# Performance work log

Measured on AMD Instinct MI355X. Metric: run time of the kernel, lower is better.

The kernel has to match this reference:

```python
import jax, jax.numpy as jnp
import numpy as np

N_HEADS = 8
WINDOW = 64
NEG = -1e9


def _layer_norm(x, g, b, eps=1e-5):
    mu = jnp.mean(x, axis=-1, keepdims=True)
    var = jnp.mean((x - mu) ** 2, axis=-1, keepdims=True)
    return g * (x - mu) / jnp.sqrt(var + eps) + b


def _sinusoidal_pe(S, D):
    pos = jnp.arange(S, dtype=jnp.float32)[:, None]
    div = jnp.exp(jnp.arange(0, D, 2, dtype=jnp.float32) * (-jnp.log(jnp.float32(10000.0)) / D))
    pe = jnp.zeros((S, D), jnp.float32)
    pe = pe.at[:, 0::2].set(jnp.sin(pos * div))
    pe = pe.at[:, 1::2].set(jnp.cos(pos * div))
    return pe


def setup_inputs():
    key = jax.random.key(0)
    ks = jax.random.split(key, 8)
    L, S, D, DFF = 4, 2048, 1024, 2048
    p = lambda k, shape: jax.random.normal(k, shape, jnp.float32) * 0.02
    return {
        "T": 1800,
        "enc_inputs": jax.random.normal(ks[0], (1, S, D), jnp.float32),
        "global_idx": jax.random.randint(ks[1], (32,), 0, 27000),
        "Wq": p(ks[2], (L, D, D)),
        "Wk": p(ks[3], (L, D, D)),
        "Wv": p(ks[4], (L, D, D)),
        "Wo": p(ks[5], (L, D, D)),
        "ln1_g": jnp.ones((L, D), jnp.float32),
        "ln1_b": jnp.zeros((L, D), jnp.float32),
        "W1": p(ks[6], (L, D, DFF)),
        "W2": p(ks[7], (L, DFF, D)),
        "ln2_g": jnp.ones((L, D), jnp.float32),
        "ln2_b": jnp.zeros((L, D), jnp.float32),
    }


def reference(T, enc_inputs, global_idx, Wq, Wk, Wv, Wo, ln1_g, ln1_b, W1, W2, ln2_g, ln2_b):
    B, S, D = enc_inputs.shape
    L = Wq.shape[0]
    H, DK = N_HEADS, D // N_HEADS

    # enc_outputs = enc_inputs + PE(enc_inputs) = 2*enc_inputs + pe (faithful to source)
    pe = _sinusoidal_pe(S, D)
    x = enc_inputs + (enc_inputs + pe[None])

    # mask vector: 1 = local token, -1 = global token, 0 = pad
    idx = jnp.arange(S)
    mvec = jnp.where(idx < T, 1.0, 0.0)
    g = global_idx // 15
    valid = (g >= 0) & (g < S)
    is_global = jnp.any((idx[None, :] == g[:, None]) & valid[:, None], axis=0)
    mvec = jnp.where(is_global, jnp.float32(-1.0), mvec)

    half = WINDOW // 2
    local = jnp.abs(idx[:, None] - idx[None, :]) <= half
    nonpad = mvec != 0.0
    glob = mvec == -1.0
    allowed = nonpad[:, None] & nonpad[None, :] & (local | glob[:, None] | glob[None, :])
    scale = 1.0 / jnp.sqrt(jnp.float32(DK))

    for l in range(L):
        # local-global multi-head self-attention
        q = (x @ Wq[l]).reshape(B, S, H, DK).transpose(0, 2, 1, 3)
        k = (x @ Wk[l]).reshape(B, S, H, DK).transpose(0, 2, 1, 3)
        v = (x @ Wv[l]).reshape(B, S, H, DK).transpose(0, 2, 1, 3)
        scores = jnp.einsum("bhqd,bhkd->bhqk", q, k) * scale
        scores = jnp.where(allowed[None, None], scores, jnp.float32(NEG))
        attn = jax.nn.softmax(scores, axis=-1)
        ctx = jnp.einsum("bhqk,bhkd->bhqd", attn, v).transpose(0, 2, 1, 3).reshape(B, S, D)
        x = _layer_norm(ctx @ Wo[l] + x, ln1_g[l], ln1_b[l])
        # position-wise FFN with residual + LayerNorm
        h = jax.nn.relu(x @ W1[l]) @ W2[l]
        x = _layer_norm(h + x, ln2_g[l], ln2_b[l])

    return x[0]  # squeeze(0): (S, D)
```

## Files before the change

### kernel.cpp

```cpp
#include <hip/hip_runtime.h>
#include <cstdint>
#include <cstddef>

#define S_LEN  2048
#define D_MODEL 1024
#define D_FF   2048
#define NLAYER 4

typedef float  f32x4  __attribute__((ext_vector_type(4)));
typedef __bf16 bf16x8 __attribute__((ext_vector_type(8)));
typedef __bf16 bf16x4 __attribute__((ext_vector_type(4)));

#define ATT_SCALE 0.08838834764831845f

__device__ __forceinline__ void async_copy16(const void* g, void* s) {
    __builtin_amdgcn_global_load_lds((const __attribute__((address_space(1))) void*)g,
                                     (__attribute__((address_space(3))) void*)s, 16, 0, 0);
}

template<int NW>
__device__ __forceinline__ float blockRedSum(float v, float* red) {
    #pragma unroll
    for (int off = 32; off > 0; off >>= 1) v += __shfl_down(v, off);
    const int t = threadIdx.x;
    if ((t & 63) == 0) red[t >> 6] = v;
    __syncthreads();
    float r = red[0];
    #pragma unroll
    for (int i = 1; i < NW; i++) r += red[i];
    __syncthreads();
    return r;
}

__global__ __launch_bounds__(256)
void init_mask_kernel(const float* __restrict__ enc, float* __restrict__ x,
                      __bf16* __restrict__ xb, const int* __restrict__ gidx,
                      int* __restrict__ isg, int* __restrict__ gcols, int* __restrict__ ngc,
                      float* __restrict__ vmean) {
    const int t = threadIdx.x;
    if (blockIdx.x < S_LEN) {
        const int s = blockIdx.x;
        #pragma unroll
        for (int i = 0; i < 4; i++) {
            const int d = t + i * 256;
            const float freq = expf(-(float)(d & ~1) * (9.210340371976184f / 1024.0f));
            const float ang = (float)s * freq;
            const float pe = (d & 1) ? cosf(ang) : sinf(ang);
            const float v = 2.0f * enc[(size_t)s * D_MODEL + d] + pe;
            x[(size_t)s * D_MODEL + d] = v;
            xb[(size_t)s * D_MODEL + d] = (__bf16)v;
        }
    } else {
        #pragma unroll
        for (int i = 0; i < 4; i++) vmean[t + i * 256] = 0.0f;
        __shared__ int gsh[32];
        __shared__ int cnt;
        if (t < 32) {
            const int g = gidx[t] / 15;
            gsh[t] = (g >= 0 && g < S_LEN) ? g : -1;
        }
        if (t == 0) cnt = 0;
        __syncthreads();
        #pragma unroll
        for (int i = 0; i < 8; i++) {
            const int s = t + i * 256;
            int f = 0;
            #pragma unroll
            for (int j = 0; j < 32; j++) f |= (gsh[j] == s) ? 1 : 0;
            isg[s] = f;
            if (f) { const int p = atomicAdd(&cnt, 1); gcols[p] = s; }
        }
        __syncthreads();
        if (t == 0) *ngc = cnt;
    }
}

__global__ __launch_bounds__(256)
void transpose_all_kernel(const float* __restrict__ Wq, const float* __restrict__ Wk,
                          const float* __restrict__ Wv, const float* __restrict__ Wo,
                          const float* __restrict__ W1, const float* __restrict__ W2,
                          __bf16* __restrict__ out) {
    const int layer = blockIdx.x >> 10;
    const int r = blockIdx.x & 1023;
    const size_t lw = (size_t)layer * 1024 * 1024;
    const size_t lf = (size_t)layer * 1024 * 2048;
    __bf16* arena = out + (size_t)layer * 8 * 1024 * 1024;
    const float* in; __bf16* o; int K, N, n0, k0;
    if (r < 512) {
        const int m = r >> 7, rr = r & 127;
        in = ((m == 0) ? Wq : (m == 1) ? Wk : (m == 2) ? Wv : Wo) + lw;
        o  = arena + (size_t)m * 1024 * 1024;
        K = 1024; N = 1024; n0 = (rr & 7) * 128; k0 = (rr >> 3) * 64;
    } else if (r < 768) {
        const int rr = r - 512;
        in = W1 + lf; o = arena + (size_t)4 * 1024 * 1024;
        K = 1024; N = 2048; n0 = (rr & 15) * 128; k0 = (rr >> 4) * 64;
    } else {
        const int rr = r - 768;
        in = W2 + lf; o = arena + (size_t)6 * 1024 * 1024;
        K = 2048; N = 1024; n0 = (rr & 7) * 128; k0 = (rr >> 3) * 64;
    }
    __shared__ __bf16 tile[128][80];
    const int t = threadIdx.x;
    {
        const int n4 = t & 31;
        const int kg = t >> 5;
        #pragma unroll
        for (int u = 0; u < 2; u++) {
            const int k4 = kg + 8 * u;
            f32x4 v[4];
            #pragma unroll
            for (int kk = 0; kk < 4; kk++)
                v[kk] = *(const f32x4*)&in[(size_t)(k0 + 4 * k4 + kk) * N + n0 + 4 * n4];
            const int cpr = ((k4 >> 1) ^ (n4 & 7)) * 2 + (k4 & 1);
            #pragma unroll
            for (int j = 0; j < 4; j++) {
                bf16x4 w;
                w[0] = (__bf16)v[0][j];
                w[1] = (__bf16)v[1][j];
                w[2] = (__bf16)v[2][j];
                w[3] = (__bf16)v[3][j];
                *(bf16x4*)&tile[4 * n4 + j][4 * cpr] = w;
            }
        }
    }
    __syncthreads();
    {
        const int p = t & 7, nb = t >> 3;
        #pragma unroll
        for (int i = 0; i < 4; i++) {
            const int n = nb + 32 * i;
            const bf16x8 vv = *(const bf16x8*)&tile[n][8 * (p ^ ((n >> 2) & 7))];
            *(bf16x8*)&o[(size_t)(n0 + n) * K + k0 + 8 * p] = vv;
        }
    }
}

template<int BM, int BN, int WSM, int WSN, int EPI, bool VACC>
__global__ __launch_bounds__(WSM * WSN * 64)
void gemm_bt(const __bf16* __restrict__ A, const __bf16* __restrict__ Bt,
             void* __restrict__ Cv, float* __restrict__ vmean, int M, int N, int K) {
    constexpr int NW = WSM * WSN, NT = NW * 64;
    constexpr int WM = BM / WSM, WN = BN / WSN;
    constexpr int MI = WM / 16, NI = WN / 16;
    constexpr int RPR = NT / 8;
    constexpr int RA = BM / RPR, RB = BN / RPR;
    __shared__ __bf16 As[2 * BM * 64];
    __shared__ __bf16 Bs[2 * BN * 64];
    const int t = threadIdx.x;
    const int w = t >> 6, l = t & 63;
    const int l15 = l & 15, q4 = l >> 4;
    const int wr = w / WSN, wc = w % WSN;
    const int m0 = blockIdx.y * BM, n0 = blockIdx.x * BN;

    const int srow = t >> 3;
    const int kc8  = (((t & 7) ^ (srow & 7)) * 8);
    const __bf16* ag = A  + (size_t)(m0 + srow) * K + kc8;
    const __bf16* bg = Bt + (size_t)(n0 + srow) * K + kc8;

    const int r7 = l15 & 7;
    int arow[MI], brow[NI];
    #pragma unroll
    for (int i = 0; i < MI; i++) arow[i] = (wr * WM + i * 16 + l15) * 64;
    #pragma unroll
    for (int j = 0; j < NI; j++) brow[j] = (wc * WN + j * 16 + l15) * 64;

    f32x4 acc[MI][NI];
    #pragma unroll
    for (int i = 0; i < MI; i++)
        #pragma unroll
        for (int j = 0; j < NI; j++) acc[i][j] = (f32x4){0.f, 0.f, 0.f, 0.f};

    auto stage = [&](int buf, int k0) {
        __bf16* ab = As + buf * (BM * 64) + w * 512;
        __bf16* bb = Bs + buf * (BN * 64) + w * 512;
        #pragma unroll
        for (int rr = 0; rr < RA; rr++)
            async_copy16(ag + (size_t)rr * RPR * K + k0, ab + rr * RPR * 64);
        #pragma unroll
        for (int rr = 0; rr < RB; rr++)
            async_copy16(bg + (size_t)rr * RPR * K + k0, bb + rr * RPR * 64);
    };
    auto compute = [&](int buf) {
        const __bf16* ab = As + buf * (BM * 64);
        const __bf16* bb = Bs + buf * (BN * 64);
        #pragma unroll
        for (int s = 0; s < 64; s += 32) {
            const int slot = ((q4 + (s >> 3)) ^ r7) * 8;
            bf16x8 af[MI], bfr[NI];
            #pragma unroll
            for (int i = 0; i < MI; i++) af[i]  = *(const bf16x8*)(ab + arow[i] + slot);
            #pragma unroll
            for (int j = 0; j < NI; j++) bfr[j] = *(const bf16x8*)(bb + brow[j] + slot);
            #pragma unroll
            for (int i = 0; i < MI; i++)
                #pragma unroll
                for (int j = 0; j < NI; j++)
                    acc[i][j] = __builtin_amdgcn_mfma_f32_16x16x32_bf16(af[i], bfr[j], acc[i][j], 0, 0, 0);
        }
    };

    stage(0, 0);
    __syncthreads();
    int cur = 0;
    int k0 = 0;
    for (; k0 + 64 < K; k0 += 64) {
        stage(cur ^ 1, k0 + 64);
        compute(cur);
        __syncthreads();
        cur ^= 1;
    }
    compute(cur);

    const int r0 = m0 + wr * WM + q4 * 4;
    const int c0 = n0 + wc * WN + l15;
    if constexpr (EPI == 0) {
        float* C = (float*)Cv;
        #pragma unroll
        for (int i = 0; i < MI; i++)
            #pragma unroll
            for (int j = 0; j < NI; j++)
                #pragma unroll
                for (int r = 0; r < 4; r++)
                    C[(size_t)(r0 + i * 16 + r) * N + c0 + j * 16] = acc[i][j][r];
    } else if constexpr (EPI == 1) {
        __bf16* C = (__bf16*)Cv;
        #pragma unroll
        for (int i = 0; i < MI; i++)
            #pragma unroll
            for (int j = 0; j < NI; j++)
                #pragma unroll
                for (int r = 0; r < 4; r++)
                    C[(size_t)(r0 + i * 16 + r) * N + c0 + j * 16] = (__bf16)fmaxf(acc[i][j][r], 0.0f);
    } else {
        __bf16* C = (__bf16*)Cv;
        #pragma unroll
        for (int i = 0; i < MI; i++)
            #pragma unroll
            for (int j = 0; j < NI; j++)
                #pragma unroll
                for (int r = 0; r < 4; r++)
                    C[(size_t)(r0 + i * 16 + r) * N + c0 + j * 16] = (__bf16)acc[i][j][r];
    }
    if constexpr (VACC) {
        #pragma unroll
        for (int j = 0; j < NI; j++) {
            const int col = c0 + j * 16;
            if (col >= 2048) {
                float s = 0.f;
                #pragma unroll
                for (int i = 0; i < MI; i++)
                    #pragma unroll
                    for (int r = 0; r < 4; r++) s += acc[i][j][r];
                s += __shfl_xor(s, 16);
                s += __shfl_xor(s, 32);
                if (q4 == 0) atomicAdd(&vmean[col - 2048], s);
            }
        }
    }
}

__global__ __launch_bounds__(256)
void attn_kernel(const __bf16* __restrict__ qkvb, const int* __restrict__ Tp,
                 const int* __restrict__ isg, const int* __restrict__ gcols,
                 const int* __restrict__ ngcp, const float* __restrict__ vmean,
                 __bf16* __restrict__ ctx, float* __restrict__ Og,
                 float* __restrict__ mg, float* __restrict__ lg) {
    const int h = blockIdx.y, hd = h * 128;
    const int t = threadIdx.x;
    const int T = *Tp, ng = *ngcp;
    __shared__ __bf16 Qs[32 * 136];
    __shared__ __bf16 Ks[128 * 136];
    __shared__ __bf16 Vs[128 * 136];
    __shared__ __bf16 Ps[32 * 136];
    __shared__ float  Ss[32 * 129];
    __shared__ int cix[128], cgf[128], rtype[32];
    __shared__ int ncs;
    const int l = t & 63, w = t >> 6;
    const int l15 = l & 15, q4 = l >> 4;
    const int nb = w * 32;

    if (blockIdx.x < 64) {
        const int qt0 = blockIdx.x * 32;
        const int wl = max(qt0 - 32, 0), wh = min(qt0 + 63, S_LEN - 1);
        if (t == 0) ncs = 0;
        if (t < 32) { const int qr = qt0 + t; rtype[t] = isg[qr] ? 1 : (qr < T ? 0 : 2); }
        __syncthreads();
        if (t <= wh - wl) {
            const int c = wl + t, gf = isg[c];
            if (c < T || gf) { const int p = atomicAdd(&ncs, 1); cix[p] = c; cgf[p] = gf; }
        }
        if (t < ng) {
            const int c = gcols[t];
            if (c < wl || c > wh) { const int p = atomicAdd(&ncs, 1); cix[p] = c; cgf[p] = 1; }
        }
        {
            const int r = t >> 3, d0 = (t & 7) * 16;
            const bf16x8* src = (const bf16x8*)(qkvb + (size_t)(qt0 + r) * 3072 + hd + d0);
            *(bf16x8*)&Qs[r * 136 + d0]     = src[0];
            *(bf16x8*)&Qs[r * 136 + d0 + 8] = src[1];
        }
        __syncthreads();
        const int nc = ncs;
        if (nc + t < 128) { cix[nc + t] = -1; cgf[nc + t] = 0; }
        {
            const int j = t >> 1, d0 = (t & 1) * 64;
            const int ci = (j < nc) ? cix[j] : -1;
            if (ci >= 0) {
                const bf16x8* kp = (const bf16x8*)(qkvb + (size_t)ci * 3072 + 1024 + hd + d0);
                const bf16x8* vp = (const bf16x8*)(qkvb + (size_t)ci * 3072 + 2048 + hd + d0);
                #pragma unroll
                for (int i = 0; i < 8; i++) {
                    *(bf16x8*)&Ks[j * 136 + d0 + i * 8] = kp[i];
                    *(bf16x8*)&Vs[j * 136 + d0 + i * 8] = vp[i];
                }
            } else {
                #pragma unroll
                for (int i = 0; i < 8; i++) {
                    *(bf16x8*)&Ks[j * 136 + d0 + i * 8] = (bf16x8)(__bf16)0.f;
                    *(bf16x8*)&Vs[j * 136 + d0 + i * 8] = (bf16x8)(__bf16)0.f;
                }
            }
        }
        __syncthreads();
        {
            f32x4 sacc[2][2];
            #pragma unroll
            for (int i = 0; i < 2; i++)
                #pragma unroll
                for (int j = 0; j < 2; j++) sacc[i][j] = (f32x4){0.f, 0.f, 0.f, 0.f};
            #pragma unroll
            for (int kk = 0; kk < 4; kk++) {
                const int k0 = kk * 32;
                bf16x8 af[2], bk[2];
                af[0] = *(const bf16x8*)&Qs[l15 * 136 + k0 + q4 * 8];
                af[1] = *(const bf16x8*)&Qs[(16 + l15) * 136 + k0 + q4 * 8];
                bk[0] = *(const bf16x8*)&Ks[(nb + l15) * 136 + k0 + q4 * 8];
                bk[1] = *(const bf16x8*)&Ks[(nb + 16 + l15) * 136 + k0 + q4 * 8];
                #pragma unroll
                for (int m2 = 0; m2 < 2; m2++)
                    #pragma unroll
                    for (int n2 = 0; n2 < 2; n2++)
                        sacc[m2][n2] = __builtin_amdgcn_mfma_f32_16x16x32_bf16(af[m2], bk[n2], sacc[m2][n2], 0, 0, 0);
            }
            #pragma unroll
            for (int m2 = 0; m2 < 2; m2++)
                #pragma unroll
                for (int n2 = 0; n2 < 2; n2++)
                    #pragma unroll
                    for (int r = 0; r < 4; r++) {
                        const int row = m2 * 16 + q4 * 4 + r;
                        const int col = nb + n2 * 16 + l15;
                        const int c = cix[col];
                        const int dd = qt0 + row - c;
                        const bool ok = (c >= 0) && (((unsigned)(dd + 32) <= 64u) || cgf[col]);
                        Ss[row * 129 + col] = ok ? sacc[m2][n2][r] * ATT_SCALE : -1e30f;
                    }
        }
        __syncthreads();
        {
            const int r = t >> 3, i = t & 7;
            float mx = -1e30f;
            for (int c = i; c < 128; c += 8) mx = fmaxf(mx, Ss[r * 129 + c]);
            #pragma unroll
            for (int off = 4; off > 0; off >>= 1) mx = fmaxf(mx, __shfl_down(mx, off, 8));
            mx = __shfl(mx, 0, 8);
            float sm = 0.f;
            for (int c = i; c < 128; c += 8) {
                const float s = Ss[r * 129 + c];
                const float p = (s > -1e29f) ? __expf(s - mx) : 0.f;
                Ss[r * 129 + c] = p;
                sm += p;
            }
            #pragma unroll
            for (int off = 4; off > 0; off >>= 1) sm += __shfl_down(sm, off, 8);
            sm = __shfl(sm, 0, 8);
            const float rl = 1.0f / fmaxf(sm, 1e-30f);
            for (int c = i; c < 128; c += 8) Ps[r * 136 + c] = (__bf16)(Ss[r * 129 + c] * rl);
        }
        __syncthreads();
        {
            f32x4 oacc[2][2];
            #pragma unroll
            for (int i = 0; i < 2; i++)
                #pragma unroll
                for (int j = 0; j < 2; j++) oacc[i][j] = (f32x4){0.f, 0.f, 0.f, 0.f};
            #pragma unroll
            for (int kk = 0; kk < 4; kk++) {
                const int k0 = kk * 32;
                bf16x8 ap[2], bv[2];
                ap[0] = *(const bf16x8*)&Ps[l15 * 136 + k0 + q4 * 8];
                ap[1] = *(const bf16x8*)&Ps[(16 + l15) * 136 + k0 + q4 * 8];
                #pragma unroll
                for (int n2 = 0; n2 < 2; n2++) {
                    const int dimn = nb + n2 * 16 + l15;
                    #pragma unroll
                    for (int jj = 0; jj < 8; jj++)
                        bv[n2][jj] = Vs[(k0 + q4 * 8 + jj) * 136 + dimn];
                }
                #pragma unroll
                for (int m2 = 0; m2 < 2; m2++)
                    #pragma unroll
                    for (int n2 = 0; n2 < 2; n2++)
                        oacc[m2][n2] = __builtin_amdgcn_mfma_f32_16x16x32_bf16(ap[m2], bv[n2], oacc[m2][n2], 0, 0, 0);
            }
            #pragma unroll
            for (int m2 = 0; m2 < 2; m2++)
                #pragma unroll
                for (int n2 = 0; n2 < 2; n2++)
                    #pragma unroll
                    for (int r = 0; r < 4; r++) {
                        const int row = m2 * 16 + q4 * 4 + r;
                        const int dim = nb + n2 * 16 + l15;
                        const int rt = rtype[row];
                        const size_t o = (size_t)(qt0 + row) * D_MODEL + hd + dim;
                        if (rt == 0)      ctx[o] = (__bf16)oacc[m2][n2][r];
                        else if (rt == 2) ctx[o] = (__bf16)(vmean[hd + dim] * (1.0f / 2048.0f));
                    }
        }
    } else {
        if (ng == 0) return;
        const int cb = blockIdx.x - 64, c0 = cb * 128;
        {
            const int r = t >> 3, d0 = (t & 7) * 16;
            if (r < ng) {
                const bf16x8* src = (const bf16x8*)(qkvb + (size_t)gcols[r] * 3072 + hd + d0);
                *(bf16x8*)&Qs[r * 136 + d0]     = src[0];
                *(bf16x8*)&Qs[r * 136 + d0 + 8] = src[1];
            } else {
                *(bf16x8*)&Qs[r * 136 + d0]     = (bf16x8)(__bf16)0.f;
                *(bf16x8*)&Qs[r * 136 + d0 + 8] = (bf16x8)(__bf16)0.f;
            }
        }
        if (t < 128) { const int c = c0 + t; cix[t] = (c < T || isg[c]) ? 1 : 0; }
        {
            const int j = t >> 1, d0 = (t & 1) * 64;
            const int ci = c0 + j;
            const bf16x8* kp = (const bf16x8*)(qkvb + (size_t)ci * 3072 + 1024 + hd + d0);
            const bf16x8* vp = (const bf16x8*)(qkvb + (size_t)ci * 3072 + 2048 + hd + d0);
            #pragma unroll
            for (int i = 0; i < 8; i++) {
                *(bf16x8*)&Ks[j * 136 + d0 + i * 8] = kp[i];
                *(bf16x8*)&Vs[j * 136 + d0 + i * 8] = vp[i];
            }
        }
        __syncthreads();
        {
            f32x4 sacc[2][2];
            #pragma unroll
            for (int i = 0; i < 2; i++)
                #pragma unroll
                for (int j = 0; j < 2; j++) sacc[i][j] = (f32x4){0.f, 0.f, 0.f, 0.f};
            #pragma unroll
            for (int kk = 0; kk < 4; kk++) {
                const int k0 = kk * 32;
                bf16x8 af[2], bk[2];
                af[0] = *(const bf16x8*)&Qs[l15 * 136 + k0 + q4 * 8];
                af[1] = *(const bf16x8*)&Qs[(16 + l15) * 136 + k0 + q4 * 8];
                bk[0] = *(const bf16x8*)&Ks[(nb + l15) * 136 + k0 + q4 * 8];
                bk[1] = *(const bf16x8*)&Ks[(nb + 16 + l15) * 136 + k0 + q4 * 8];
                #pragma unroll
                for (int m2 = 0; m2 < 2; m2++)
                    #pragma unroll
                    for (int n2 = 0; n2 < 2; n2++)
                        sacc[m2][n2] = __builtin_amdgcn_mfma_f32_16x16x32_bf16(af[m2], bk[n2], sacc[m2][n2], 0, 0, 0);
            }
            #pragma unroll
            for (int m2 = 0; m2 < 2; m2++)
                #pragma unroll
                for (int n2 = 0; n2 < 2; n2++)
                    #pragma unroll
                    for (int r = 0; r < 4; r++) {
                        const int row = m2 * 16 + q4 * 4 + r;
                        const int col = nb + n2 * 16 + l15;
                        Ss[row * 129 + col] = cix[col] ? sacc[m2][n2][r] * ATT_SCALE : -1e30f;
                    }
        }
        __syncthreads();
        {
            const int r = t >> 3, i = t & 7;
            float mx = -1e30f;
            for (int c = i; c < 128; c += 8) mx = fmaxf(mx, Ss[r * 129 + c]);
            #pragma unroll
            for (int off = 4; off > 0; off >>= 1) mx = fmaxf(mx, __shfl_down(mx, off, 8));
            mx = __shfl(mx, 0, 8);
            float sm = 0.f;
            for (int c = i; c < 128; c += 8) {
                const float s = Ss[r * 129 + c];
                const float p = (s > -1e29f) ? __expf(s - mx) : 0.f;
                Ps[r * 136 + c] = (__bf16)p;
                sm += p;
            }
            #pragma unroll
            for (int off = 4; off > 0; off >>= 1) sm += __shfl_down(sm, off, 8);
            if (i == 0) { mg[(h * 16 + cb) * 32 + r] = mx; lg[(h * 16 + cb) * 32 + r] = sm; }
        }
        __syncthreads();
        {
            f32x4 oacc[2][2];
            #pragma unroll
            for (int i = 0; i < 2; i++)
                #pragma unroll
                for (int j = 0; j < 2; j++) oacc[i][j] = (f32x4){0.f, 0.f, 0.f, 0.f};
            #pragma unroll
            for (int kk = 0; kk < 4; kk++) {
                const int k0 = kk * 32;
                bf16x8 ap[2], bv[2];
                ap[0] = *(const bf16x8*)&Ps[l15 * 136 + k0 + q4 * 8];
                ap[1] = *(const bf16x8*)&Ps[(16 + l15) * 136 + k0 + q4 * 8];
                #pragma unroll
                for (int n2 = 0; n2 < 2; n2++) {
                    const int dimn = nb + n2 * 16 + l15;
                    #pragma unroll
                    for (int jj = 0; jj < 8; jj++)
                        bv[n2][jj] = Vs[(k0 + q4 * 8 + jj) * 136 + dimn];
                }
                #pragma unroll
                for (int m2 = 0; m2 < 2; m2++)
                    #pragma unroll
                    for (int n2 = 0; n2 < 2; n2++)
                        oacc[m2][n2] = __builtin_amdgcn_mfma_f32_16x16x32_bf16(ap[m2], bv[n2], oacc[m2][n2], 0, 0, 0);
            }
            #pragma unroll
            for (int m2 = 0; m2 < 2; m2++)
                #pragma unroll
                for (int n2 = 0; n2 < 2; n2++)
                    #pragma unroll
                    for (int r = 0; r < 4; r++) {
                        const int row = m2 * 16 + q4 * 4 + r;
                        const int dim = nb + n2 * 16 + l15;
                        Og[((size_t)(h * 16 + cb) * 32 + row) * 128 + dim] = oacc[m2][n2][r];
                    }
        }
    }
}

__global__ __launch_bounds__(256)
void attn_gcomb(const int* __restrict__ gcols, const int* __restrict__ ngcp,
                const float* __restrict__ Og, const float* __restrict__ mg,
                const float* __restrict__ lg, __bf16* __restrict__ ctx) {
    const int h = blockIdx.x, hd = h * 128, t = threadIdx.x;
    const int ng = *ngcp;
    const int r = t >> 3, i = t & 7;
    if (r >= ng) return;
    float M = -1e30f;
    #pragma unroll
    for (int cb = 0; cb < 16; cb++) M = fmaxf(M, mg[(h * 16 + cb) * 32 + r]);
    float e[16], L = 0.f;
    #pragma unroll
    for (int cb = 0; cb < 16; cb++) {
        e[cb] = __expf(mg[(h * 16 + cb) * 32 + r] - M);
        L += e[cb] * lg[(h * 16 + cb) * 32 + r];
    }
    const float rL = 1.0f / fmaxf(L, 1e-30f);
    const int grow = gcols[r];
    for (int d = i; d < 128; d += 8) {
        float o = 0.f;
        #pragma unroll
        for (int cb = 0; cb < 16; cb++)
            o += e[cb] * Og[((size_t)(h * 16 + cb) * 32 + r) * 128 + d];
        ctx[(size_t)grow * D_MODEL + hd + d] = (__bf16)(o * rL);
    }
}

__global__ __launch_bounds__(256)
void ln_kernel(const float* __restrict__ y, const float* __restrict__ r,
               const float* __restrict__ g, const float* __restrict__ b,
               float* __restrict__ xo, __bf16* __restrict__ xb, float* __restrict__ vz) {
    const int row = blockIdx.x, t = threadIdx.x;
    if (vz != nullptr && row == 0) {
        #pragma unroll
        for (int i = 0; i < 4; i++) vz[t + i * 256] = 0.0f;
    }
    const float* yr = y + (size_t)row * D_MODEL;
    const float* rr = r + (size_t)row * D_MODEL;
    __shared__ float red[4];
    float v[4]; float s = 0.f;
    #pragma unroll
    for (int i = 0; i < 4; i++) { const int d = t + i * 256; v[i] = yr[d] + rr[d]; s += v[i]; }
    s = blockRedSum<4>(s, red);
    const float mu = s * (1.0f / 1024.0f);
    float vs = 0.f;
    #pragma unroll
    for (int i = 0; i < 4; i++) { const float dd = v[i] - mu; vs += dd * dd; }
    vs = blockRedSum<4>(vs, red);
    const float rstd = rsqrtf(vs * (1.0f / 1024.0f) + 1e-5f);
    #pragma unroll
    for (int i = 0; i < 4; i++) {
        const int d = t + i * 256;
        const float o = g[d] * (v[i] - mu) * rstd + b[d];
        xo[(size_t)row * D_MODEL + d] = o;
        xb[(size_t)row * D_MODEL + d] = (__bf16)o;
    }
}

extern "C" void kernel_launch(void* const* d_in, const int* in_sizes, int n_in,
                              void* d_out, int out_size, void* d_ws, size_t ws_size,
                              hipStream_t stream) {
    const int*   Tp   = (const int*)  d_in[0];
    const float* enc  = (const float*)d_in[1];
    const int*   gidx = (const int*)  d_in[2];
    const float* Wq   = (const float*)d_in[3];
    const float* Wk   = (const float*)d_in[4];
    const float* Wv   = (const float*)d_in[5];
    const float* Wo   = (const float*)d_in[6];
    const float* ln1g = (const float*)d_in[7];
    const float* ln1b = (const float*)d_in[8];
    const float* W1   = (const float*)d_in[9];
    const float* W2   = (const float*)d_in[10];
    const float* ln2g = (const float*)d_in[11];
    const float* ln2b = (const float*)d_in[12];

    char* p = (char*)d_ws;
    size_t off = 0;
    auto alloc = [&](size_t bytes) -> void* {
        void* q = p + off;
        off += (bytes + 255) & ~(size_t)255;
        return q;
    };
    float*  x     = (float*) alloc((size_t)S_LEN * D_MODEL * 4);
    __bf16* xb    = (__bf16*)alloc((size_t)S_LEN * D_MODEL * 2);
    __bf16* qkvb  = (__bf16*)alloc((size_t)S_LEN * 3072 * 2);
    __bf16* ctx   = (__bf16*)alloc((size_t)S_LEN * D_MODEL * 2);
    float*  g1    = (float*) alloc((size_t)S_LEN * D_MODEL * 4);
    __bf16* h1    = (__bf16*)alloc((size_t)S_LEN * D_FF * 2);
    __bf16* wT    = (__bf16*)alloc((size_t)4 * 8 * 1024 * 1024 * 2);
    float*  vmean = (float*) alloc(1024 * 4);
    int*    isg   = (int*)   alloc(S_LEN * 4);
    int*    gcols = (int*)   alloc(S_LEN * 4);
    int*    ngc   = (int*)   alloc(256);
    float*  Og    = (float*) alloc((size_t)8 * 16 * 32 * 128 * 4);
    float*  mgb   = (float*) alloc(8 * 16 * 32 * 4);
    float*  lgb   = (float*) alloc(8 * 16 * 32 * 4);

    init_mask_kernel<<<S_LEN + 1, 256, 0, stream>>>(enc, x, xb, gidx, isg, gcols, ngc, vmean);
    transpose_all_kernel<<<4096, 256, 0, stream>>>(Wq, Wk, Wv, Wo, W1, W2, wT);

    for (int l = 0; l < NLAYER; l++) {
        __bf16* wL = wT + (size_t)l * 8 * 1024 * 1024;
        gemm_bt<64, 128, 1, 2, 2, true><<<dim3(24, 32), 128, 0, stream>>>(xb, wL, (void*)qkvb, vmean, S_LEN, 3072, 1024);

        attn_kernel<<<dim3(80, 8), 256, 0, stream>>>(qkvb, Tp, isg, gcols, ngc, vmean, ctx, Og, mgb, lgb);
        attn_gcomb<<<8, 256, 0, stream>>>(gcols, ngc, Og, mgb, lgb, ctx);

        gemm_bt<64, 64, 2, 2, 0, false><<<dim3(16, 32), 256, 0, stream>>>(ctx, wL + (size_t)3 * 1024 * 1024, (void*)g1, nullptr, S_LEN, 1024, 1024);
        ln_kernel<<<S_LEN, 256, 0, stream>>>(g1, x, ln1g + l * 1024, ln1b + l * 1024, x, xb, nullptr);

        gemm_bt<64, 128, 2, 2, 1, false><<<dim3(16, 32), 256, 0, stream>>>(xb, wL + (size_t)4 * 1024 * 1024, (void*)h1, nullptr, S_LEN, 2048, 1024);
        gemm_bt<64, 64, 2, 2, 0, false><<<dim3(16, 32), 256, 0, stream>>>(h1, wL + (size_t)6 * 1024 * 1024, (void*)g1, nullptr, S_LEN, 1024, 2048);
        float* xout = (l == NLAYER - 1) ? (float*)d_out : x;
        ln_kernel<<<S_LEN, 256, 0, stream>>>(g1, x, ln2g + l * 1024, ln2b + l * 1024, xout, xb, vmean);
    }
}
```

Baseline: 702.8 us.

## Keep Q and softmax scores in registers in attention; widen QKV GEMM block

```diff
diff --git a/kernel.cpp b/kernel.cpp
--- a/kernel.cpp
+++ b/kernel.cpp
@@ -269,19 +269,24 @@
     const int h = blockIdx.y, hd = h * 128;
     const int t = threadIdx.x;
     const int T = *Tp, ng = *ngcp;
-    __shared__ __bf16 Qs[32 * 136];
     __shared__ __bf16 Ks[128 * 136];
     __shared__ __bf16 Vs[128 * 136];
     __shared__ __bf16 Ps[32 * 136];
-    __shared__ float  Ss[32 * 129];
+    __shared__ float  wmax[4 * 32];
+    __shared__ float  wsum[4 * 32];
     __shared__ int cix[128], cgf[128], rtype[32];
     __shared__ int ncs;
     const int l = t & 63, w = t >> 6;
     const int l15 = l & 15, q4 = l >> 4;
     const int nb = w * 32;
 
-    if (blockIdx.x < 64) {
-        const int qt0 = blockIdx.x * 32;
+    const bool isLocal = (blockIdx.x < 64);
+    if (!isLocal && ng == 0) return;
+
+    bf16x8 qreg[2][4];
+    int qt0 = 0, cb = 0;
+    if (isLocal) {
+        qt0 = blockIdx.x * 32;
         const int wl = max(qt0 - 32, 0), wh = min(qt0 + 63, S_LEN - 1);
         if (t == 0) ncs = 0;
         if (t < 32) { const int qr = qt0 + t; rtype[t] = isg[qr] ? 1 : (qr < T ? 0 : 2); }
@@ -294,12 +299,11 @@
             const int c = gcols[t];
             if (c < wl || c > wh) { const int p = atomicAdd(&ncs, 1); cix[p] = c; cgf[p] = 1; }
         }
-        {
-            const int r = t >> 3, d0 = (t & 7) * 16;
-            const bf16x8* src = (const bf16x8*)(qkvb + (size_t)(qt0 + r) * 3072 + hd + d0);
-            *(bf16x8*)&Qs[r * 136 + d0]     = src[0];
-            *(bf16x8*)&Qs[r * 136 + d0 + 8] = src[1];
-        }
+        #pragma unroll
+        for (int m2 = 0; m2 < 2; m2++)
+            #pragma unroll
+            for (int kk = 0; kk < 4; kk++)
+                qreg[m2][kk] = *(const bf16x8*)(qkvb + (size_t)(qt0 + m2 * 16 + l15) * 3072 + hd + kk * 32 + q4 * 8);
         __syncthreads();
         const int nc = ncs;
         if (nc + t < 128) { cix[nc + t] = -1; cgf[nc + t] = 0; }
@@ -322,115 +326,16 @@
                 }
             }
         }
-        __syncthreads();
-        {
-            f32x4 sacc[2][2];
-            #pragma unroll
-            for (int i = 0; i < 2; i++)
-                #pragma unroll
-                for (int j = 0; j < 2; j++) sacc[i][j] = (f32x4){0.f, 0.f, 0.f, 0.f};
-            #pragma unroll
-            for (int kk = 0; kk < 4; kk++) {
-                const int k0 = kk * 32;
-                bf16x8 af[2], bk[2];
-                af[0] = *(const bf16x8*)&Qs[l15 * 136 + k0 + q4 * 8];
-                af[1] = *(const bf16x8*)&Qs[(16 + l15) * 136 + k0 + q4 * 8];
-                bk[0] = *(const bf16x8*)&Ks[(nb + l15) * 136 + k0 + q4 * 8];
-                bk[1] = *(const bf16x8*)&Ks[(nb + 16 + l15) * 136 + k0 + q4 * 8];
-                #pragma unroll
-                for (int m2 = 0; m2 < 2; m2++)
-                    #pragma unroll
-                    for (int n2 = 0; n2 < 2; n2++)
-                        sacc[m2][n2] = __builtin_amdgcn_mfma_f32_16x16x32_bf16(af[m2], bk[n2], sacc[m2][n2], 0, 0, 0);
-            }
-            #pragma unroll
-            for (int m2 = 0; m2 < 2; m2++)
-                #pragma unroll
-                for (int n2 = 0; n2 < 2; n2++)
-                    #pragma unroll
-                    for (int r = 0; r < 4; r++) {
-                        const int row = m2 * 16 + q4 * 4 + r;
-                        const int col = nb + n2 * 16 + l15;
-                        const int c = cix[col];
-                        const int dd = qt0 + row - c;
-                        const bool ok = (c >= 0) && (((unsigned)(dd + 32) <= 64u) || cgf[col]);
-                        Ss[row * 129 + col] = ok ? sacc[m2][n2][r] * ATT_SCALE : -1e30f;
-                    }
-        }
-        __syncthreads();
-        {
-            const int r = t >> 3, i = t & 7;
-            float mx = -1e30f;
-            for (int c = i; c < 128; c += 8) mx = fmaxf(mx, Ss[r * 129 + c]);
-            #pragma unroll
-            for (int off = 4; off > 0; off >>= 1) mx = fmaxf(mx, __shfl_down(mx, off, 8));
-            mx = __shfl(mx, 0, 8);
-            float sm = 0.f;
-            for (int c = i; c < 128; c += 8) {
-                const float s = Ss[r * 129 + c];
-                const float p = (s > -1e29f) ? __expf(s - mx) : 0.f;
-                Ss[r * 129 + c] = p;
-                sm += p;
-            }
-            #pragma unroll
-            for (int off = 4; off > 0; off >>= 1) sm += __shfl_down(sm, off, 8);
-            sm = __shfl(sm, 0, 8);
-            const float rl = 1.0f / fmaxf(sm, 1e-30f);
-            for (int c = i; c < 128; c += 8) Ps[r * 136 + c] = (__bf16)(Ss[r * 129 + c] * rl);
-        }
-        __syncthreads();
-        {
-            f32x4 oacc[2][2];
-            #pragma unroll
-            for (int i = 0; i < 2; i++)
-                #pragma unroll
-                for (int j = 0; j < 2; j++) oacc[i][j] = (f32x4){0.f, 0.f, 0.f, 0.f};
-            #pragma unroll
-            for (int kk = 0; kk < 4; kk++) {
-                const int k0 = kk * 32;
-                bf16x8 ap[2], bv[2];
-                ap[0] = *(const bf16x8*)&Ps[l15 * 136 + k0 + q4 * 8];
-                ap[1] = *(const bf16x8*)&Ps[(16 + l15) * 136 + k0 + q4 * 8];
-                #pragma unroll
-                for (int n2 = 0; n2 < 2; n2++) {
-                    const int dimn = nb + n2 * 16 + l15;
-                    #pragma unroll
-                    for (int jj = 0; jj < 8; jj++)
-                        bv[n2][jj] = Vs[(k0 + q4 * 8 + jj) * 136 + dimn];
-                }
-                #pragma unroll
-                for (int m2 = 0; m2 < 2; m2++)
-                    #pragma unroll
-                    for (int n2 = 0; n2 < 2; n2++)
-                        oacc[m2][n2] = __builtin_amdgcn_mfma_f32_16x16x32_bf16(ap[m2], bv[n2], oacc[m2][n2], 0, 0, 0);
-            }
-            #pragma unroll
-            for (int m2 = 0; m2 < 2; m2++)
-                #pragma unroll
-                for (int n2 = 0; n2 < 2; n2++)
-                    #pragma unroll
-                    for (int r = 0; r < 4; r++) {
-                        const int row = m2 * 16 + q4 * 4 + r;
-                        const int dim = nb + n2 * 16 + l15;
-                        const int rt = rtype[row];
-                        const size_t o = (size_t)(qt0 + row) * D_MODEL + hd + dim;
-                        if (rt == 0)      ctx[o] = (__bf16)oacc[m2][n2][r];
-                        else if (rt == 2) ctx[o] = (__bf16)(vmean[hd + dim] * (1.0f / 2048.0f));
-                    }
-        }
     } else {
-        if (ng == 0) return;
-        const int cb = blockIdx.x - 64, c0 = cb * 128;
-        {
-            const int r = t >> 3, d0 = (t & 7) * 16;
-            if (r < ng) {
-                const bf16x8* src = (const bf16x8*)(qkvb + (size_t)gcols[r] * 3072 + hd + d0);
-                *(bf16x8*)&Qs[r * 136 + d0]     = src[0];
-                *(bf16x8*)&Qs[r * 136 + d0 + 8] = src[1];
-            } else {
-                *(bf16x8*)&Qs[r * 136 + d0]     = (bf16x8)(__bf16)0.f;
-                *(bf16x8*)&Qs[r * 136 + d0 + 8] = (bf16x8)(__bf16)0.f;
-            }
+        cb = blockIdx.x - 64;
+        const int c0 = cb * 128;
+        #pragma unroll
+        for (int m2 = 0; m2 < 2; m2++) {
+            const int ri = m2 * 16 + l15;
+            const int qrow = (ri < ng) ? gcols[ri] : 0;
+            #pragma unroll
+            for (int kk = 0; kk < 4; kk++)
+                qreg[m2][kk] = *(const bf16x8*)(qkvb + (size_t)qrow * 3072 + hd + kk * 32 + q4 * 8);
         }
         if (t < 128) { const int c = c0 + t; cix[t] = (c < T || isg[c]) ? 1 : 0; }
         {
@@ -444,94 +349,162 @@
                 *(bf16x8*)&Vs[j * 136 + d0 + i * 8] = vp[i];
             }
         }
-        __syncthreads();
-        {
-            f32x4 sacc[2][2];
-            #pragma unroll
-            for (int i = 0; i < 2; i++)
-                #pragma unroll
-                for (int j = 0; j < 2; j++) sacc[i][j] = (f32x4){0.f, 0.f, 0.f, 0.f};
-            #pragma unroll
-            for (int kk = 0; kk < 4; kk++) {
-                const int k0 = kk * 32;
-                bf16x8 af[2], bk[2];
-                af[0] = *(const bf16x8*)&Qs[l15 * 136 + k0 + q4 * 8];
-                af[1] = *(const bf16x8*)&Qs[(16 + l15) * 136 + k0 + q4 * 8];
-                bk[0] = *(const bf16x8*)&Ks[(nb + l15) * 136 + k0 + q4 * 8];
-                bk[1] = *(const bf16x8*)&Ks[(nb + 16 + l15) * 136 + k0 + q4 * 8];
-                #pragma unroll
-                for (int m2 = 0; m2 < 2; m2++)
-                    #pragma unroll
-                    for (int n2 = 0; n2 < 2; n2++)
-                        sacc[m2][n2] = __builtin_amdgcn_mfma_f32_16x16x32_bf16(af[m2], bk[n2], sacc[m2][n2], 0, 0, 0);
+    }
+    __syncthreads();
+
+    f32x4 sacc[2][2];
+    #pragma unroll
+    for (int i = 0; i < 2; i++)
+        #pragma unroll
+        for (int j = 0; j < 2; j++) sacc[i][j] = (f32x4){0.f, 0.f, 0.f, 0.f};
+    __builtin_amdgcn_s_setprio(1);
+    #pragma unroll
+    for (int kk = 0; kk < 4; kk++) {
+        const int k0 = kk * 32;
+        bf16x8 bk[2];
+        bk[0] = *(const bf16x8*)&Ks[(nb + l15) * 136 + k0 + q4 * 8];
+        bk[1] = *(const bf16x8*)&Ks[(nb + 16 + l15) * 136 + k0 + q4 * 8];
+        #pragma unroll
+        for (int m2 = 0; m2 < 2; m2++)
+            #pragma unroll
+            for (int n2 = 0; n2 < 2; n2++)
+                sacc[m2][n2] = __builtin_amdgcn_mfma_f32_16x16x32_bf16(qreg[m2][kk], bk[n2], sacc[m2][n2], 0, 0, 0);
+    }
+    __builtin_amdgcn_s_setprio(0);
+
+    float sv[2][2][4];
+    #pragma unroll
+    for (int m2 = 0; m2 < 2; m2++)
+        #pragma unroll
+        for (int n2 = 0; n2 < 2; n2++)
+            #pragma unroll
+            for (int r = 0; r < 4; r++) {
+                const int col = nb + n2 * 16 + l15;
+                bool ok;
+                if (isLocal) {
+                    const int row = m2 * 16 + q4 * 4 + r;
+                    const int c = cix[col];
+                    const int dd = qt0 + row - c;
+                    ok = (c >= 0) && (((unsigned)(dd + 32) <= 64u) || cgf[col]);
+                } else {
+                    ok = cix[col] != 0;
+                }
+                sv[m2][n2][r] = ok ? sacc[m2][n2][r] * ATT_SCALE : -1e30f;
             }
-            #pragma unroll
-            for (int m2 = 0; m2 < 2; m2++)
+
+    #pragma unroll
+    for (int m2 = 0; m2 < 2; m2++)
+        #pragma unroll
+        for (int r = 0; r < 4; r++) {
+            float m = fmaxf(sv[m2][0][r], sv[m2][1][r]);
+            #pragma unroll
+            for (int msk = 1; msk <= 8; msk <<= 1) m = fmaxf(m, __shfl_xor(m, msk));
+            if (l15 == 0) wmax[w * 32 + m2 * 16 + q4 * 4 + r] = m;
+        }
+    __syncthreads();
+    float gmx[2][4];
+    #pragma unroll
+    for (int m2 = 0; m2 < 2; m2++)
+        #pragma unroll
+        for (int r = 0; r < 4; r++) {
+            const int row = m2 * 16 + q4 * 4 + r;
+            float m = wmax[row];
+            #pragma unroll
+            for (int wi = 1; wi < 4; wi++) m = fmaxf(m, wmax[wi * 32 + row]);
+            gmx[m2][r] = m;
+        }
+
+    #pragma unroll
+    for (int m2 = 0; m2 < 2; m2++)
+        #pragma unroll
+        for (int r = 0; r < 4; r++) {
+            #pragma unroll
+            for (int n2 = 0; n2 < 2; n2++) {
+                const float s = sv[m2][n2][r];
+                sv[m2][n2][r] = (s > -1e29f) ? __expf(s - gmx[m2][r]) : 0.f;
+            }
+            float sm = sv[m2][0][r] + sv[m2][1][r];
+            #pragma unroll
+            for (int msk = 1; msk <= 8; msk <<= 1) sm += __shfl_xor(sm, msk);
+            if (l15 == 0) wsum[w * 32 + m2 * 16 + q4 * 4 + r] = sm;
+        }
+    __syncthreads();
+
+    #pragma unroll
+    for (int m2 = 0; m2 < 2; m2++)
+        #pragma unroll
+        for (int r = 0; r < 4; r++) {
+            const int row = m2 * 16 + q4 * 4 + r;
+            float sm = wsum[row] + wsum[32 + row] + wsum[64 + row] + wsum[96 + row];
+            if (isLocal) {
+                const float rl = 1.0f / fmaxf(sm, 1e-30f);
                 #pragma unroll
                 for (int n2 = 0; n2 < 2; n2++)
-                    #pragma unroll
-                    for (int r = 0; r < 4; r++) {
-                        const int row = m2 * 16 + q4 * 4 + r;
-                        const int col = nb + n2 * 16 + l15;
-                        Ss[row * 129 + col] = cix[col] ? sacc[m2][n2][r] * ATT_SCALE : -1e30f;
-                    }
-        }
-        __syncthreads();
-        {
-            const int r = t >> 3, i = t & 7;
-            float mx = -1e30f;
-            for (int c = i; c < 128; c += 8) mx = fmaxf(mx, Ss[r * 129 + c]);
-            #pragma unroll
-            for (int off = 4; off > 0; off >>= 1) mx = fmaxf(mx, __shfl_down(mx, off, 8));
-            mx = __shfl(mx, 0, 8);
-            float sm = 0.f;
-            for (int c = i; c < 128; c += 8) {
-                const float s = Ss[r * 129 + c];
-                const float p = (s > -1e29f) ? __expf(s - mx) : 0.f;
-                Ps[r * 136 + c] = (__bf16)p;
-                sm += p;
+                    Ps[row * 136 + nb + n2 * 16 + l15] = (__bf16)(sv[m2][n2][r] * rl);
+            } else {
+                if (w == 0 && l15 == 0) {
+                    mg[(h * 16 + cb) * 32 + row] = gmx[m2][r];
+                    lg[(h * 16 + cb) * 32 + row] = sm;
+                }
+                #pragma unroll
+                for (int n2 = 0; n2 < 2; n2++)
+                    Ps[row * 136 + nb + n2 * 16 + l15] = (__bf16)sv[m2][n2][r];
             }
-            #pragma unroll
-            for (int off = 4; off > 0; off >>= 1) sm += __shfl_down(sm, off, 8);
-            if (i == 0) { mg[(h * 16 + cb) * 32 + r] = mx; lg[(h * 16 + cb) * 32 + r] = sm; }
-        }
-        __syncthreads();
-        {
-            f32x4 oacc[2][2];
-            #pragma unroll
-            for (int i = 0; i < 2; i++)
-                #pragma unroll
-                for (int j = 0; j < 2; j++) oacc[i][j] = (f32x4){0.f, 0.f, 0.f, 0.f};
-            #pragma unroll
-            for (int kk = 0; kk < 4; kk++) {
-                const int k0 = kk * 32;
-                bf16x8 ap[2], bv[2];
-                ap[0] = *(const bf16x8*)&Ps[l15 * 136 + k0 + q4 * 8];
-                ap[1] = *(const bf16x8*)&Ps[(16 + l15) * 136 + k0 + q4 * 8];
-                #pragma unroll
-                for (int n2 = 0; n2 < 2; n2++) {
-                    const int dimn = nb + n2 * 16 + l15;
-                    #pragma unroll
-                    for (int jj = 0; jj < 8; jj++)
-                        bv[n2][jj] = Vs[(k0 + q4 * 8 + jj) * 136 + dimn];
+        }
+    __syncthreads();
+
+    f32x4 oacc[2][2];
+    #pragma unroll
+    for (int i = 0; i < 2; i++)
+        #pragma unroll
+        for (int j = 0; j < 2; j++) oacc[i][j] = (f32x4){0.f, 0.f, 0.f, 0.f};
+    #pragma unroll
+    for (int kk = 0; kk < 4; kk++) {
+        const int k0 = kk * 32;
+        bf16x8 ap[2], bv[2];
+        ap[0] = *(const bf16x8*)&Ps[l15 * 136 + k0 + q4 * 8];
+        ap[1] = *(const bf16x8*)&Ps[(16 + l15) * 136 + k0 + q4 * 8];
+        #pragma unroll
+        for (int n2 = 0; n2 < 2; n2++) {
+            const int dimn = nb + n2 * 16 + l15;
+            #pragma unroll
+            for (int jj = 0; jj < 8; jj++)
+                bv[n2][jj] = Vs[(k0 + q4 * 8 + jj) * 136 + dimn];
+        }
+        __builtin_amdgcn_s_setprio(1);
+        #pragma unroll
+        for (int m2 = 0; m2 < 2; m2++)
+            #pragma unroll
+            for (int n2 = 0; n2 < 2; n2++)
+                oacc[m2][n2] = __builtin_amdgcn_mfma_f32_16x16x32_bf16(ap[m2], bv[n2], oacc[m2][n2], 0, 0, 0);
+        __builtin_amdgcn_s_setprio(0);
+    }
+
+    if (isLocal) {
+        #pragma unroll
+        for (int m2 = 0; m2 < 2; m2++)
+            #pragma unroll
+            for (int n2 = 0; n2 < 2; n2++)
+                #pragma unroll
+                for (int r = 0; r < 4; r++) {
+                    const int row = m2 * 16 + q4 * 4 + r;
+                    const int dim = nb + n2 * 16 + l15;
+                    const int rt = rtype[row];
+                    const size_t o = (size_t)(qt0 + row) * D_MODEL + hd + dim;
+                    if (rt == 0)      ctx[o] = (__bf16)oacc[m2][n2][r];
+                    else if (rt == 2) ctx[o] = (__bf16)(vmean[hd + dim] * (1.0f / 2048.0f));
                 }
-                #pragma unroll
-                for (int m2 = 0; m2 < 2; m2++)
-                    #pragma unroll
-                    for (int n2 = 0; n2 < 2; n2++)
-                        oacc[m2][n2] = __builtin_amdgcn_mfma_f32_16x16x32_bf16(ap[m2], bv[n2], oacc[m2][n2], 0, 0, 0);
-            }
-            #pragma unroll
-            for (int m2 = 0; m2 < 2; m2++)
-                #pragma unroll
-                for (int n2 = 0; n2 < 2; n2++)
-                    #pragma unroll
-                    for (int r = 0; r < 4; r++) {
-                        const int row = m2 * 16 + q4 * 4 + r;
-                        const int dim = nb + n2 * 16 + l15;
-                        Og[((size_t)(h * 16 + cb) * 32 + row) * 128 + dim] = oacc[m2][n2][r];
-                    }
-        }
+    } else {
+        #pragma unroll
+        for (int m2 = 0; m2 < 2; m2++)
+            #pragma unroll
+            for (int n2 = 0; n2 < 2; n2++)
+                #pragma unroll
+                for (int r = 0; r < 4; r++) {
+                    const int row = m2 * 16 + q4 * 4 + r;
+                    const int dim = nb + n2 * 16 + l15;
+                    Og[((size_t)(h * 16 + cb) * 32 + row) * 128 + dim] = oacc[m2][n2][r];
+                }
     }
 }
 
@@ -638,7 +611,7 @@
 
     for (int l = 0; l < NLAYER; l++) {
         __bf16* wL = wT + (size_t)l * 8 * 1024 * 1024;
-        gemm_bt<64, 128, 1, 2, 2, true><<<dim3(24, 32), 128, 0, stream>>>(xb, wL, (void*)qkvb, vmean, S_LEN, 3072, 1024);
+        gemm_bt<64, 128, 2, 2, 2, true><<<dim3(24, 32), 256, 0, stream>>>(xb, wL, (void*)qkvb, vmean, S_LEN, 3072, 1024);
 
         attn_kernel<<<dim3(80, 8), 256, 0, stream>>>(qkvb, Tp, isg, gcols, ngc, vmean, ctx, Og, mgb, lgb);
         attn_gcomb<<<8, 256, 0, stream>>>(gcols, ngc, Og, mgb, lgb, ctx);
```

After: 666.5 us. 5.2% less time.
